# Kernel optimization log

Hardware: AMD Instinct MI355X
Metric: run time of the kernel (lower is better)

Reference implementation:

```python
import jax, jax.numpy as jnp
import numpy as np

IN, H, B = 1024, 1024, 8192


def _uniform(key, shape, stdv):
    return jax.random.uniform(key, shape, jnp.float32, -stdv, stdv)


def setup_inputs() -> dict:
    key = jax.random.key(0)
    ks = jax.random.split(key, 20)
    stdv = 1.0 / np.sqrt(H)
    inp = {
        "x": jax.random.normal(ks[0], (B, IN), jnp.float32),
        "h": jax.random.normal(ks[1], (B, H), jnp.float32),
        "c": jax.random.normal(ks[2], (B, H), jnp.float32),
        # fused input->gates weight [IN, 4H] (gate order: I, F, G, O) and bias [4H]
        "Wi": _uniform(ks[3], (IN, 4 * H), stdv),
        "bi": _uniform(ks[4], (4 * H,), stdv),
        # fused hidden->gates weight [H, 4H] and bias [4H]
        "Wh": _uniform(ks[5], (H, 4 * H), stdv),
        "bh": _uniform(ks[6], (4 * H,), stdv),
    }
    return inp


def reference(x, h, c, Wi, bi, Wh, bh):
    # Two fused GEMMs replacing the 8 separate nn.Linear calls (same math).
    gates = x @ Wi + bi + h @ Wh + bh  # [B, 4H]
    gI, gF, gG, gO = jnp.split(gates, 4, axis=-1)
    I = jax.nn.sigmoid(gI)
    F = jax.nn.sigmoid(gF)
    G = jnp.tanh(gG)   # nlF = Tanh
    O = jax.nn.sigmoid(gO)
    c_ = F * c + I * G
    h_ = O * jnp.tanh(c_)  # nlF2 = Tanh
    return (h_, c_)
```

## Files before the change

kernel.cpp:

```cpp
#include <hip/hip_runtime.h>
#include <stdint.h>

#define IN_DIM 1024
#define H_DIM  1024
#define BATCH  8192
#define KDIM   2048
#define NDIM   4096
#define BM     256
#define BN     256
#define BK     64
#define NT     (KDIM / BK)

typedef __bf16 bf16x8 __attribute__((ext_vector_type(8)));
typedef float  f32x4  __attribute__((ext_vector_type(4)));
typedef unsigned int u32;

static __device__ __forceinline__ unsigned short f2bf(float f) {
  u32 u = __builtin_bit_cast(u32, f);
  u += 0x7FFFu + ((u >> 16) & 1u);
  return (unsigned short)(u >> 16);
}

static __device__ __forceinline__ float sigm(float x) {
  return 1.0f / (1.0f + __expf(-x));
}
static __device__ __forceinline__ float tanh_fast(float x) {
  float e = __expf(-2.0f * fabsf(x));
  float t = (1.0f - e) / (1.0f + e);
  return copysignf(t, x);
}

__global__ void conv_a(const float* __restrict__ x, const float* __restrict__ h,
                       unsigned short* __restrict__ A) {
  const int total = BATCH * KDIM / 4;
  for (int i = blockIdx.x * blockDim.x + threadIdx.x; i < total;
       i += gridDim.x * blockDim.x) {
    int b = i >> 9;
    int k = (i & 511) << 2;
    const float* src = (k < IN_DIM) ? (x + (size_t)b * IN_DIM + k)
                                    : (h + (size_t)b * H_DIM + (k - IN_DIM));
    float4 v = *reinterpret_cast<const float4*>(src);
    ushort4 o;
    o.x = f2bf(v.x); o.y = f2bf(v.y); o.z = f2bf(v.z); o.w = f2bf(v.w);
    *reinterpret_cast<ushort4*>(A + (size_t)b * KDIM + k) = o;
  }
}

__global__ void conv_b(const float* __restrict__ Wi, const float* __restrict__ Wh,
                       unsigned short* __restrict__ Bt) {
  __shared__ float tile[32][33];
  int k0 = blockIdx.x * 32;
  int c0 = blockIdx.y * 32;
  int tx = threadIdx.x;
  int ty = threadIdx.y;
  const float* src = (k0 < IN_DIM) ? (Wi + (size_t)k0 * NDIM)
                                   : (Wh + (size_t)(k0 - IN_DIM) * NDIM);
  for (int i = 0; i < 4; i++) {
    int r = ty + 8 * i;
    tile[r][tx] = src[(size_t)r * NDIM + c0 + tx];
  }
  __syncthreads();
  int g = c0 >> 10;
  int ubase = c0 & 1023;
  for (int i = 0; i < 4; i++) {
    int cc = ty + 8 * i;
    int j = 4 * (ubase + cc) + g;
    Bt[(size_t)j * KDIM + k0 + tx] = f2bf(tile[tx][cc]);
  }
}

__global__ void conv_bias(const float* __restrict__ bi, const float* __restrict__ bh,
                          float* __restrict__ bias) {
  int j = blockIdx.x * blockDim.x + threadIdx.x;
  if (j < NDIM) {
    int c = ((j & 3) << 10) + (j >> 2);
    bias[j] = bi[c] + bh[c];
  }
}

static __device__ __forceinline__ void gload_lds16(const void* g, void* l) {
  __builtin_amdgcn_global_load_lds(
      (const __attribute__((address_space(1))) u32*)g,
      (__attribute__((address_space(3))) u32*)l, 16, 0, 0);
}

#define MFMA __builtin_amdgcn_mfma_f32_16x16x32_bf16

__launch_bounds__(512, 2)
__global__ void lstm_gemm(const unsigned short* __restrict__ A,
                          const unsigned short* __restrict__ Bt,
                          const float* __restrict__ bias,
                          const float* __restrict__ Cin,
                          float* __restrict__ Hout,
                          float* __restrict__ Cout) {
  __shared__ __align__(16) char smem[131072];

  const int t  = threadIdx.x;
  const int l  = t & 63;
  const int w  = t >> 6;
  const int lane16 = l & 15;
  const int kg = l >> 4;
  const int wr = w >> 2;
  const int wc = w & 3;

  int bid = blockIdx.x;
  int swz = (bid & 7) * 64 + (bid >> 3);
  int brow = (swz >> 4) * BM;
  int bcol = (swz & 15) * BN;

  int slot0 = w * 128 + l, slot1 = slot0 + 64;
  int rih0 = slot0 >> 3, rih1 = slot1 >> 3;
  int c0 = (slot0 & 7) ^ (rih0 & 7), c1 = (slot1 & 7) ^ (rih1 & 7);

  const unsigned short* a0q0 = A + (size_t)(brow + (rih0 >> 6) * 128 + (rih0 & 63)) * KDIM + c0 * 8;
  const unsigned short* a0q1 = A + (size_t)(brow + (rih1 >> 6) * 128 + (rih1 & 63)) * KDIM + c1 * 8;
  const unsigned short* a1q0 = a0q0 + 131072;
  const unsigned short* a1q1 = a0q1 + 131072;
  const unsigned short* b0q0 = Bt + (size_t)(bcol + (rih0 >> 5) * 64 + (rih0 & 31)) * KDIM + c0 * 8;
  const unsigned short* b0q1 = Bt + (size_t)(bcol + (rih1 >> 5) * 64 + (rih1 & 31)) * KDIM + c1 * 8;
  const unsigned short* b1q0 = b0q0 + 65536;
  const unsigned short* b1q1 = b0q1 + 65536;

#define GL(gp, loff) gload_lds16((gp), smem + (loff) + w * 2048 + l * 16)

  const int msk = (lane16 & 7) << 4;
  char* vA0 = smem + wr * 8192 + lane16 * 128 + ((kg * 16) ^ msk);
  char* vA1 = smem + wr * 8192 + lane16 * 128 + ((64 + kg * 16) ^ msk);
  char* vB0 = smem + 65536 + wc * 4096 + lane16 * 128 + ((kg * 16) ^ msk);
  char* vB1 = smem + 65536 + wc * 4096 + lane16 * 128 + ((64 + kg * 16) ^ msk);

  f32x4 acc[8][4];
#pragma unroll
  for (int m = 0; m < 8; m++)
#pragma unroll
    for (int n = 0; n < 4; n++) acc[m][n] = (f32x4){0.f, 0.f, 0.f, 0.f};

  GL(a0q0, 0);                 GL(a0q1, 1024);
  GL(b0q0, 65536);             GL(b0q1, 65536 + 1024);
  GL(a1q0, 16384);             GL(a1q1, 16384 + 1024);
  GL(b1q0, 65536 + 16384);     GL(b1q1, 65536 + 16384 + 1024);
  GL(a0q0 + 64, 32768);        GL(a0q1 + 64, 32768 + 1024);
  GL(b0q0 + 64, 65536 + 32768);GL(b0q1 + 64, 65536 + 32768 + 1024);
  GL(a1q0 + 64, 32768 + 16384);GL(a1q1 + 64, 32768 + 16384 + 1024);
  asm volatile("s_waitcnt vmcnt(6)" ::: "memory");
  __builtin_amdgcn_s_barrier();
  a0q0 += 128; a0q1 += 128; a1q0 += 128; a1q1 += 128;
  b0q0 += 128; b0q1 += 128; b1q0 += 64;  b1q1 += 64;

  bf16x8 afr[4][2], bfr[4][2];

#define BODY(P)                                                              \
  {                                                                          \
    \
    _Pragma("unroll") for (int mm = 0; mm < 4; mm++) {                       \
      afr[mm][0] = *(const bf16x8*)(vA0 + (P)*32768 + mm*2048);              \
      afr[mm][1] = *(const bf16x8*)(vA1 + (P)*32768 + mm*2048);              \
    }                                                                        \
    _Pragma("unroll") for (int nn = 0; nn < 2; nn++) {                       \
      bfr[nn][0] = *(const bf16x8*)(vB0 + (P)*32768 + nn*2048);              \
      bfr[nn][1] = *(const bf16x8*)(vB1 + (P)*32768 + nn*2048);              \
    }                                                                        \
    GL(b1q0, 65536 + ((P)^1)*32768 + 16384);                                 \
    GL(b1q1, 65536 + ((P)^1)*32768 + 16384 + 1024);                          \
    __builtin_amdgcn_s_barrier();                                            \
    asm volatile("s_waitcnt lgkmcnt(0)" ::: "memory");                       \
    __builtin_amdgcn_s_setprio(1);                                           \
    _Pragma("unroll") for (int mm = 0; mm < 4; mm++)                         \
      _Pragma("unroll") for (int nn = 0; nn < 2; nn++) {                     \
        acc[mm][nn] = MFMA(afr[mm][0], bfr[nn][0], acc[mm][nn], 0, 0, 0);    \
        acc[mm][nn] = MFMA(afr[mm][1], bfr[nn][1], acc[mm][nn], 0, 0, 0);    \
      }                                                                      \
    __builtin_amdgcn_s_setprio(0);                                           \
    __builtin_amdgcn_s_barrier();                                            \
                     \
    _Pragma("unroll") for (int nn = 2; nn < 4; nn++) {                       \
      bfr[nn][0] = *(const bf16x8*)(vB0 + (P)*32768 + 16384 + (nn-2)*2048);  \
      bfr[nn][1] = *(const bf16x8*)(vB1 + (P)*32768 + 16384 + (nn-2)*2048);  \
    }                                                                        \
    GL(a0q0, (P)*32768);                                                     \
    GL(a0q1, (P)*32768 + 1024);                                              \
    __builtin_amdgcn_s_barrier();                                            \
    asm volatile("s_waitcnt lgkmcnt(0)" ::: "memory");                       \
    __builtin_amdgcn_s_setprio(1);                                           \
    _Pragma("unroll") for (int mm = 0; mm < 4; mm++)                         \
      _Pragma("unroll") for (int nn = 2; nn < 4; nn++) {                     \
        acc[mm][nn] = MFMA(afr[mm][0], bfr[nn][0], acc[mm][nn], 0, 0, 0);    \
        acc[mm][nn] = MFMA(afr[mm][1], bfr[nn][1], acc[mm][nn], 0, 0, 0);    \
      }                                                                      \
    __builtin_amdgcn_s_setprio(0);                                           \
    __builtin_amdgcn_s_barrier();                                            \
                     \
    _Pragma("unroll") for (int mm = 0; mm < 4; mm++) {                       \
      afr[mm][0] = *(const bf16x8*)(vA0 + (P)*32768 + 16384 + mm*2048);      \
      afr[mm][1] = *(const bf16x8*)(vA1 + (P)*32768 + 16384 + mm*2048);      \
    }                                                                        \
    GL(b0q0, 65536 + (P)*32768);                                             \
    GL(b0q1, 65536 + (P)*32768 + 1024);                                      \
    __builtin_amdgcn_s_barrier();                                            \
    asm volatile("s_waitcnt lgkmcnt(0)" ::: "memory");                       \
    __builtin_amdgcn_s_setprio(1);                                           \
    _Pragma("unroll") for (int mm = 0; mm < 4; mm++)                         \
      _Pragma("unroll") for (int nn = 0; nn < 2; nn++) {                     \
        acc[4+mm][nn] = MFMA(afr[mm][0], bfr[nn][0], acc[4+mm][nn], 0, 0, 0);\
        acc[4+mm][nn] = MFMA(afr[mm][1], bfr[nn][1], acc[4+mm][nn], 0, 0, 0);\
      }                                                                      \
    __builtin_amdgcn_s_setprio(0);                                           \
    __builtin_amdgcn_s_barrier();                                            \
       \
    GL(a1q0, (P)*32768 + 16384);                                             \
    GL(a1q1, (P)*32768 + 16384 + 1024);                                      \
    asm volatile("s_waitcnt vmcnt(6)" ::: "memory");                         \
    __builtin_amdgcn_s_barrier();                                            \
    __builtin_amdgcn_s_setprio(1);                                           \
    _Pragma("unroll") for (int mm = 0; mm < 4; mm++)                         \
      _Pragma("unroll") for (int nn = 2; nn < 4; nn++) {                     \
        acc[4+mm][nn] = MFMA(afr[mm][0], bfr[nn][0], acc[4+mm][nn], 0, 0, 0);\
        acc[4+mm][nn] = MFMA(afr[mm][1], bfr[nn][1], acc[4+mm][nn], 0, 0, 0);\
      }                                                                      \
    __builtin_amdgcn_s_setprio(0);                                           \
    __builtin_amdgcn_s_barrier();                                            \
    a0q0 += 64; a0q1 += 64; a1q0 += 64; a1q1 += 64;                          \
    b0q0 += 64; b0q1 += 64; b1q0 += 64; b1q1 += 64;                          \
  }

  for (int it = 0; it < NT / 2; ++it) {
    BODY(0)
    BODY(1)
  }
#undef BODY
#undef GL

  asm volatile("s_waitcnt vmcnt(0)" ::: "memory");
  __builtin_amdgcn_s_barrier();

  float bv[4];
#pragma unroll
  for (int nn = 0; nn < 4; nn++)
    bv[nn] = bias[bcol + wc * 64 + nn * 16 + lane16];

  float* Gep = (float*)(smem + (size_t)w * 4352);

#pragma unroll
  for (int m = 0; m < 8; m++) {
#pragma unroll
    for (int nn = 0; nn < 4; nn++)
#pragma unroll
      for (int r = 0; r < 4; r++)
        Gep[(kg * 4 + r) * 68 + nn * 16 + lane16] = acc[m][nn][r] + bv[nn];
    asm volatile("s_waitcnt lgkmcnt(0)" ::: "memory");
#pragma unroll
    for (int p = 0; p < 4; p++) {
      int row = p * 4 + kg;
      const float4 g4 = *(const float4*)(Gep + row * 68 + lane16 * 4);
      int R = brow + wr * 128 + m * 16 + row;
      int U = (bcol >> 2) + wc * 16 + lane16;
      float Ig = sigm(g4.x);
      float Fg = sigm(g4.y);
      float Gg = tanh_fast(g4.z);
      float Og = sigm(g4.w);
      size_t idx = (size_t)R * H_DIM + U;
      float cv = Cin[idx];
      float cn = Fg * cv + Ig * Gg;
      Hout[idx] = Og * tanh_fast(cn);
      Cout[idx] = cn;
    }
    asm volatile("s_waitcnt lgkmcnt(0)" ::: "memory");
  }
}

extern "C" void kernel_launch(void* const* d_in, const int* in_sizes, int n_in,
                              void* d_out, int out_size, void* d_ws, size_t ws_size,
                              hipStream_t stream) {
  const float* x  = (const float*)d_in[0];
  const float* h  = (const float*)d_in[1];
  const float* c  = (const float*)d_in[2];
  const float* Wi = (const float*)d_in[3];
  const float* bi = (const float*)d_in[4];
  const float* Wh = (const float*)d_in[5];
  const float* bh = (const float*)d_in[6];

  float* out  = (float*)d_out;
  float* Hout = out;
  float* Cout = out + (size_t)BATCH * H_DIM;

  unsigned short* Abf = (unsigned short*)d_ws;
  unsigned short* Btb = (unsigned short*)((char*)d_ws + 33554432);
  float*          bsf = (float*)((char*)d_ws + 50331648);

  conv_a<<<2048, 256, 0, stream>>>(x, h, Abf);
  conv_b<<<dim3(64, 128), dim3(32, 8), 0, stream>>>(Wi, Wh, Btb);
  conv_bias<<<16, 256, 0, stream>>>(bi, bh, bsf);
  lstm_gemm<<<512, 512, 0, stream>>>(Abf, Btb, bsf, c, Hout, Cout);
}
```

Before: 162.6 us.

## Permute gate columns so epilogue reads all four gates from registers

Changes the column interleaving of the converted weight and bias so that each lane's four 16-wide N subtiles correspond to the I, F, G, O gates of the same hidden unit. The epilogue can then compute the LSTM cell directly from accumulator registers without staging gates through shared memory. It also prefetches the c input and the bias into registers before the main loop, overlapping those loads with the GEMM. This removes the LDS round trip and its barriers in the epilogue, at the cost of 36 extra live registers during the main loop (with launch_bounds 512,2) and narrower per-lane global stores.

```diff
diff --git a/kernel.cpp b/kernel.cpp
--- a/kernel.cpp
+++ b/kernel.cpp
@@ -64,7 +64,8 @@
   int ubase = c0 & 1023;
   for (int i = 0; i < 4; i++) {
     int cc = ty + 8 * i;
-    int j = 4 * (ubase + cc) + g;
+    int u = ubase + cc;
+    int j = ((u >> 4) << 6) + (g << 4) + (u & 15);
     Bt[(size_t)j * KDIM + k0 + tx] = f2bf(tile[tx][cc]);
   }
 }
@@ -73,7 +74,9 @@
                           float* __restrict__ bias) {
   int j = blockIdx.x * blockDim.x + threadIdx.x;
   if (j < NDIM) {
-    int c = ((j & 3) << 10) + (j >> 2);
+    int u = ((j >> 6) << 4) + (j & 15);
+    int g = (j >> 4) & 3;
+    int c = (g << 10) + u;
     bias[j] = bi[c] + bh[c];
   }
 }
@@ -134,6 +137,19 @@
   for (int m = 0; m < 8; m++)
 #pragma unroll
     for (int n = 0; n < 4; n++) acc[m][n] = (f32x4){0.f, 0.f, 0.f, 0.f};
+
+  const int U = (bcol >> 2) + wc * 16 + lane16;
+  const float* cinp = Cin + (size_t)(brow + wr * 128 + kg * 4) * H_DIM + U;
+  float cin[32];
+#pragma unroll
+  for (int m = 0; m < 8; m++)
+#pragma unroll
+    for (int r = 0; r < 4; r++)
+      cin[m * 4 + r] = cinp[(size_t)(m * 16 + r) * H_DIM];
+  float bv[4];
+#pragma unroll
+  for (int nn = 0; nn < 4; nn++)
+    bv[nn] = bias[bcol + wc * 64 + nn * 16 + lane16];
 
   GL(a0q0, 0);                 GL(a0q1, 1024);
   GL(b0q0, 65536);             GL(b0q1, 65536 + 1024);
@@ -230,42 +246,23 @@
 #undef BODY
 #undef GL
 
+  float* hp = Hout + (size_t)(brow + wr * 128 + kg * 4) * H_DIM + U;
+  float* cp = Cout + (size_t)(brow + wr * 128 + kg * 4) * H_DIM + U;
+#pragma unroll
+  for (int m = 0; m < 8; m++)
+#pragma unroll
+    for (int r = 0; r < 4; r++) {
+      float Ig = sigm(acc[m][0][r] + bv[0]);
+      float Fg = sigm(acc[m][1][r] + bv[1]);
+      float Gg = tanh_fast(acc[m][2][r] + bv[2]);
+      float Og = sigm(acc[m][3][r] + bv[3]);
+      float cn = Fg * cin[m * 4 + r] + Ig * Gg;
+      size_t off = (size_t)(m * 16 + r) * H_DIM;
+      hp[off] = Og * tanh_fast(cn);
+      cp[off] = cn;
+    }
+
   asm volatile("s_waitcnt vmcnt(0)" ::: "memory");
-  __builtin_amdgcn_s_barrier();
-
-  float bv[4];
-#pragma unroll
-  for (int nn = 0; nn < 4; nn++)
-    bv[nn] = bias[bcol + wc * 64 + nn * 16 + lane16];
-
-  float* Gep = (float*)(smem + (size_t)w * 4352);
-
-#pragma unroll
-  for (int m = 0; m < 8; m++) {
-#pragma unroll
-    for (int nn = 0; nn < 4; nn++)
-#pragma unroll
-      for (int r = 0; r < 4; r++)
-        Gep[(kg * 4 + r) * 68 + nn * 16 + lane16] = acc[m][nn][r] + bv[nn];
-    asm volatile("s_waitcnt lgkmcnt(0)" ::: "memory");
-#pragma unroll
-    for (int p = 0; p < 4; p++) {
-      int row = p * 4 + kg;
-      const float4 g4 = *(const float4*)(Gep + row * 68 + lane16 * 4);
-      int R = brow + wr * 128 + m * 16 + row;
-      int U = (bcol >> 2) + wc * 16 + lane16;
-      float Ig = sigm(g4.x);
-      float Fg = sigm(g4.y);
-      float Gg = tanh_fast(g4.z);
-      float Og = sigm(g4.w);
-      size_t idx = (size_t)R * H_DIM + U;
-      float cv = Cin[idx];
-      float cn = Fg * cv + Ig * Gg;
-      Hout[idx] = Og * tanh_fast(cn);
-      Cout[idx] = cn;
-    }
-    asm volatile("s_waitcnt lgkmcnt(0)" ::: "memory");
-  }
 }
 
 extern "C" void kernel_launch(void* const* d_in, const int* in_sizes, int n_in,
```

New measurement: 178.6 us. 1.1x slower.
